# Kernel optimization log

Hardware: AMD Instinct MI355X
Metric: run time of the kernel (lower is better)

Reference implementation:

```python
import jax, jax.numpy as jnp
import numpy as np

B, S, H = 8, 512, 1024          # batch, seq, hidden_size
E = 1024                        # moe_intermediate_size
NEXP, TOPK = 32, 4              # num_experts, top_k_experts
CAP = 512
NH = 4                          # heads in StandardAttentionExpert
HD = E // NH                    # head_dim = 256


def setup_inputs() -> dict:
    key = jax.random.key(0)
    ks = jax.random.split(key, 8)
    def init(k, shape, fan_in):
        return jax.random.normal(k, shape, jnp.float32) / np.sqrt(fan_in)
    return {
        "hidden_states": jax.random.normal(ks[0], (B, S, H), jnp.float32),
        "router_w": init(ks[1], (NEXP, H), H),            # Linear(H, NEXP, bias=False)
        "qkv_w": init(ks[2], (NEXP, 3 * E, H), H),
        "qkv_b": init(ks[3], (NEXP, 3 * E), H),
        "sw_w": init(ks[4], (NEXP, 2 * E, E), E),         # SwiGLU.w
        "sw_b": jnp.zeros((NEXP, 2 * E), jnp.float32),
        "sv_w": init(ks[5], (NEXP, E, E), E),             # SwiGLU.v
        "sv_b": jnp.zeros((NEXP, E), jnp.float32),
        "proj_w": init(ks[6], (NEXP, H, E), E),
        "proj_b": jnp.zeros((NEXP, H), jnp.float32),
    }


def _expert(x, valid, is_linear, qkv_w, qkv_b, sw_w, sw_b, sv_w, sv_b, proj_w, proj_b):
    # x: [CAP, H] padded token group for one expert; valid: [CAP] bool
    qkv = x @ qkv_w.T + qkv_b                      # [CAP, 3E]
    q, k, v = jnp.split(qkv, 3, axis=-1)           # each [CAP, E]
    vm = valid.astype(x.dtype)[:, None]
    # --- LinearAttentionExpert: group-global linear attention ---
    km, vmv = k * vm, v * vm                       # zero out padding keys/values
    kv = km.T @ vmv                                # [E, E]
    z = 1.0 / (q @ km.sum(0) + 1e-6)               # [CAP]
    lin_out = (q @ kv) * z[:, None]                # [CAP, E]
    # --- StandardAttentionExpert: 4-head softmax attention over the group ---
    qh = q.reshape(CAP, NH, HD)
    kh = k.reshape(CAP, NH, HD)
    vh = v.reshape(CAP, NH, HD)
    logits = jnp.einsum('qhd,khd->hqk', qh, kh) / np.sqrt(HD)
    logits = jnp.where(valid[None, None, :], logits, -1e9)
    attn = jax.nn.softmax(logits, axis=-1)
    std_out = jnp.einsum('hqk,khd->qhd', attn, vh).reshape(CAP, E)
    a = jnp.where(is_linear, lin_out, std_out)
    # SwiGLU then projection back to hidden size
    hgl = a @ sw_w.T + sw_b                        # [CAP, 2E]
    u, gate = jnp.split(hgl, 2, axis=-1)
    s = (u * jax.nn.silu(gate)) @ sv_w.T + sv_b    # [CAP, E]
    return s @ proj_w.T + proj_b                   # [CAP, H]


def _forward(hidden_states, router_w, qkv_w, qkv_b, sw_w, sw_b, sv_w, sv_b, proj_w, proj_b):
    T = B * S
    x = hidden_states.reshape(T, H)
    probs = jax.nn.softmax(x @ router_w.T, axis=-1)        # [T, NEXP]
    topw, topi = jax.lax.top_k(probs, TOPK)                # [T, TOPK]
    topw = topw / (topw.sum(-1, keepdims=True) + 1e-6)
    is_linear = (jnp.arange(NEXP) % 4 == 0)
    run = jax.vmap(_expert, in_axes=(0,) * 12 if False else (0, 0, 0, 0, 0, 0, 0, 0, 0, 0, 0))
    out = jnp.zeros_like(x)
    for kk in range(TOPK):
        eid = topi[:, kk]                                  # [T] expert id per token
        oh = (eid[:, None] == jnp.arange(NEXP)).astype(jnp.int32)
        pos = jnp.take_along_axis(jnp.cumsum(oh, axis=0), eid[:, None], axis=1)[:, 0] - 1
        ok = pos < CAP                                     # capacity-drop guard (CAP sized to avoid drops)
        p = jnp.where(ok, pos, CAP)                        # overflow rows land in scratch slot CAP
        buf = jnp.zeros((NEXP, CAP + 1, H), x.dtype).at[eid, p].set(x)[:, :CAP]
        vbuf = jnp.zeros((NEXP, CAP + 1), bool).at[eid, p].set(True)[:, :CAP]
        eo = run(buf, vbuf, is_linear, qkv_w, qkv_b, sw_w, sw_b, sv_w, sv_b, proj_w, proj_b)
        y = jnp.where(ok[:, None], eo[eid, jnp.minimum(pos, CAP - 1)], 0.0)
        out = out + y * topw[:, kk:kk + 1]
    return out.reshape(B, S, H)


def reference(hidden_states, router_w, qkv_w, qkv_b, sw_w, sw_b, sv_w, sv_b, proj_w, proj_b):
    return _forward(hidden_states, router_w, qkv_w, qkv_b, sw_w, sw_b, sv_w, sv_b, proj_w, proj_b)
```

## Files before the change

kernel.cpp:

```cpp
#include <hip/hip_runtime.h>
#include <hip/hip_bf16.h>
#include <cstdint>

#define T_TOK 4096
#define NEXP  32
#define TOPK  4
#define CAP   512
#define H     1024
#define E     1024
#define NH    4
#define HD    256
#define MAXROWS (T_TOK*TOPK)

typedef __attribute__((ext_vector_type(4))) float f32x4;
typedef __attribute__((ext_vector_type(8))) short short8;

__device__ __forceinline__ float bf2f(ushort u) {
  return __uint_as_float(((uint)u) << 16);
}
__device__ __forceinline__ ushort f2bf(float f) {
  uint u = __float_as_uint(f);
  uint r = (u + 0x7fffu + ((u >> 16) & 1u)) >> 16;
  return (ushort)r;
}
__device__ __forceinline__ void split2(float v, ushort& h, ushort& l) {
  h = f2bf(v);
  l = f2bf(v - bf2f(h));
}
__device__ __forceinline__ void gload16(const void* g, void* l) {
  __builtin_amdgcn_global_load_lds((const __attribute__((address_space(1))) void*)g,
                                   (__attribute__((address_space(3))) void*)l, 16, 0, 0);
}

#define CVTPK(F0, F1, HP, LP) do { \
  asm("v_cvt_pk_bf16_f32 %0, %1, %2" : "=v"(HP) : "v"(F0), "v"(F1)); \
  float _h0 = __uint_as_float((HP) << 16); \
  float _h1 = __uint_as_float((HP) & 0xffff0000u); \
  float _l0 = (F0) - _h0, _l1 = (F1) - _h1; \
  asm("v_cvt_pk_bf16_f32 %0, %1, %2" : "=v"(LP) : "v"(_l0), "v"(_l1)); \
} while (0)

#define CVTPK_HI(F0, F1, HP) \
  asm("v_cvt_pk_bf16_f32 %0, %1, %2" : "=v"(HP) : "v"(F0), "v"(F1))

__global__ __launch_bounds__(256) void k_router(const float* __restrict__ x, const float* __restrict__ rw,
                                                int* __restrict__ topi, float* __restrict__ topw) {
  int t = blockIdx.x;
  __shared__ float4 xs[256];
  __shared__ float lg[NEXP];
  const float4* xr = (const float4*)(x + (size_t)t * H);
  xs[threadIdx.x] = xr[threadIdx.x];
  __syncthreads();
  int g = threadIdx.x >> 3, s = threadIdx.x & 7;
  const float4* wr = (const float4*)(rw + (size_t)g * H);
  float acc = 0.f;
  for (int j = s; j < 256; j += 8) {
    float4 a = xs[j], b = wr[j];
    acc += a.x * b.x + a.y * b.y + a.z * b.z + a.w * b.w;
  }
  acc += __shfl_xor(acc, 1);
  acc += __shfl_xor(acc, 2);
  acc += __shfl_xor(acc, 4);
  if (s == 0) lg[g] = acc;
  __syncthreads();
  if (threadIdx.x == 0) {
    float mx = -3e38f;
    for (int j = 0; j < NEXP; j++) mx = fmaxf(mx, lg[j]);
    float p[NEXP]; float sum = 0.f;
    for (int j = 0; j < NEXP; j++) { p[j] = __expf(lg[j] - mx); sum += p[j]; }
    float inv = 1.f / sum;
    int idx[TOPK]; float val[TOPK];
    for (int k = 0; k < TOPK; k++) {
      int best = 0; float bv = -1.f;
      for (int j = 0; j < NEXP; j++) if (p[j] > bv) { bv = p[j]; best = j; }
      idx[k] = best; val[k] = bv * inv; p[best] = -2.f;
    }
    float wsn = val[0] + val[1] + val[2] + val[3] + 1e-6f;
    for (int k = 0; k < TOPK; k++) { topi[t*TOPK + k] = idx[k]; topw[t*TOPK + k] = val[k] / wsn; }
  }
}

__global__ __launch_bounds__(256) void k_scan(const int* __restrict__ topi, int* __restrict__ pos_arr,
                                              int* __restrict__ cnt_raw) {
  int p = blockIdx.x;
  int e = p >> 2, kk = p & 3;
  __shared__ int wtot[4];
  int lane = threadIdx.x & 63, wid = threadIdx.x >> 6;
  int base = 0;
  for (int t0 = 0; t0 < T_TOK; t0 += 256) {
    int t = t0 + threadIdx.x;
    bool flag = (topi[t*TOPK + kk] == e);
    unsigned long long m = __ballot(flag);
    int excl = __popcll(m & ((1ull << lane) - 1ull));
    if (lane == 0) wtot[wid] = __popcll(m);
    __syncthreads();
    int wexcl = 0, tot = 0;
#pragma unroll
    for (int w2 = 0; w2 < 4; w2++) { int v = wtot[w2]; if (w2 < wid) wexcl += v; tot += v; }
    if (flag) pos_arr[t*TOPK + kk] = base + wexcl + excl;
    base += tot;
    __syncthreads();
  }
  if (threadIdx.x == 0) cnt_raw[p] = base;
}

__global__ void k_offsets(const int* __restrict__ cnt_raw, int* __restrict__ cnt,
                          int* __restrict__ row_base, int* __restrict__ meta) {
  if (threadIdx.x == 0 && blockIdx.x == 0) {
    int acc = 0;
    for (int p = 0; p < NEXP*TOPK; p++) {
      int c = cnt_raw[p]; if (c > CAP) c = CAP;
      cnt[p] = c; row_base[p] = acc; acc += c;
    }
    meta[0] = acc;
  }
}

__global__ __launch_bounds__(256) void k_gather(const float* __restrict__ x, const int* __restrict__ topi,
                                                const int* __restrict__ pos_arr, const int* __restrict__ row_base,
                                                int* __restrict__ row_of, ushort* __restrict__ xhi, ushort* __restrict__ xlo) {
  int b = blockIdx.x;
  int t = b >> 2, kk = b & 3;
  int e = topi[b];
  int pos = pos_arr[b];
  int row = (pos < CAP) ? (row_base[e*TOPK + kk] + pos) : -1;
  if (threadIdx.x == 0) row_of[b] = row;
  if (row >= 0) {
    float4 v = ((const float4*)x)[(size_t)t * 256 + threadIdx.x];
    ushort4 h, l;
    split2(v.x, h.x, l.x); split2(v.y, h.y, l.y);
    split2(v.z, h.z, l.z); split2(v.w, h.w, l.w);
    ((ushort4*)xhi)[(size_t)row * 256 + threadIdx.x] = h;
    ((ushort4*)xlo)[(size_t)row * 256 + threadIdx.x] = l;
  }
}

template<int OMODE>
__global__ __launch_bounds__(256) void k_mfma_gemm(
    const ushort* __restrict__ Ahi, const ushort* __restrict__ Alo,
    const float* __restrict__ W, const float* __restrict__ Bias, int Ntot, int n0c,
    float* __restrict__ Cf, ushort* __restrict__ Chi, ushort* __restrict__ Clo, int ldc,
    const int* __restrict__ row_base, const int* __restrict__ cnt, const int* __restrict__ meta) {
  int e = blockIdx.z;
  bool full = (e & 3) == 0;
  int rs = row_base[e*4];
  int re = row_base[e*4 + 3] + cnt[e*4 + 3];
  int m0 = rs + blockIdx.y * 128;
  if (m0 >= re) return;
  int nb = blockIdx.x * 128;
  int tot = meta[0];
  __shared__ ushort ldsA[2][128*32];
  __shared__ float  ldsW[128*32];
  int tid = threadIdx.x;
  int lane = tid & 63, w = tid >> 6;
  int wr = w >> 1, wc = w & 1;
  int lr = lane & 15, lk = lane >> 4;
  f32x4 acc[4][4] = {};

  int r0 = tid >> 2;
  int gA = (tid >> 3) & 3;
  int kc = (((tid & 3) ^ gA)) << 3;
  size_t a_off0 = (size_t)min(m0 + r0, tot - 1) * 1024 + kc;
  size_t a_off1 = (size_t)min(m0 + 64 + r0, tot - 1) * 1024 + kc;
  uint d0 = (uint)tid * 8, d1 = (uint)(256 + tid) * 8;

  const float* wsrc0; const float* wsrc1; const float* wsrc2; const float* wsrc3;
  {
    int i0 = tid;           int rr0 = i0 >> 3, c0 = (i0 & 7) ^ (rr0 & 7);
    int i1 = tid + 256;     int rr1 = i1 >> 3, c1 = (i1 & 7) ^ (rr1 & 7);
    int i2 = tid + 512;     int rr2 = i2 >> 3, c2 = (i2 & 7) ^ (rr2 & 7);
    int i3 = tid + 768;     int rr3 = i3 >> 3, c3 = (i3 & 7) ^ (rr3 & 7);
    wsrc0 = W + ((size_t)e * Ntot + n0c + nb + rr0) * 1024 + c0 * 4;
    wsrc1 = W + ((size_t)e * Ntot + n0c + nb + rr1) * 1024 + c1 * 4;
    wsrc2 = W + ((size_t)e * Ntot + n0c + nb + rr2) * 1024 + c2 * 4;
    wsrc3 = W + ((size_t)e * Ntot + n0c + nb + rr3) * 1024 + c3 * 4;
  }

  for (int kb = 0; kb < 1024; kb += 32) {
    gload16(Ahi + a_off0 + kb, &ldsA[0][d0]);
    gload16(Ahi + a_off1 + kb, &ldsA[0][d1]);
    if (full) {
      gload16(Alo + a_off0 + kb, &ldsA[1][d0]);
      gload16(Alo + a_off1 + kb, &ldsA[1][d1]);
    }
    gload16(wsrc0 + kb, &ldsW[(uint)tid * 4]);
    gload16(wsrc1 + kb, &ldsW[(uint)(tid + 256) * 4]);
    gload16(wsrc2 + kb, &ldsW[(uint)(tid + 512) * 4]);
    gload16(wsrc3 + kb, &ldsW[(uint)(tid + 768) * 4]);
    __syncthreads();
    short8 ah[4], al[4], bh[4], bl[4];
#pragma unroll
    for (int m = 0; m < 4; m++) {
      int rA = wr*64 + m*16 + lr;
      int sA = (lk ^ ((rA >> 1) & 3)) << 3;
      ah[m] = *(const short8*)&ldsA[0][rA*32 + sA];
    }
    if (full) {
#pragma unroll
      for (int m = 0; m < 4; m++) {
        int rA = wr*64 + m*16 + lr;
        int sA = (lk ^ ((rA >> 1) & 3)) << 3;
        al[m] = *(const short8*)&ldsA[1][rA*32 + sA];
      }
#pragma unroll
      for (int n = 0; n < 4; n++) {
        int rB = wc*64 + n*16 + lr;
        int x7 = rB & 7;
        float4 w0 = *(const float4*)&ldsW[rB*32 + (((lk*2)     ^ x7) << 2)];
        float4 w1 = *(const float4*)&ldsW[rB*32 + (((lk*2 + 1) ^ x7) << 2)];
        uint hp0, hp1, hp2, hp3, lp0, lp1, lp2, lp3;
        CVTPK(w0.x, w0.y, hp0, lp0);
        CVTPK(w0.z, w0.w, hp1, lp1);
        CVTPK(w1.x, w1.y, hp2, lp2);
        CVTPK(w1.z, w1.w, hp3, lp3);
        uint4 hv = make_uint4(hp0, hp1, hp2, hp3);
        uint4 lv = make_uint4(lp0, lp1, lp2, lp3);
        bh[n] = __builtin_bit_cast(short8, hv);
        bl[n] = __builtin_bit_cast(short8, lv);
      }
#pragma unroll
      for (int m = 0; m < 4; m++)
#pragma unroll
        for (int n = 0; n < 4; n++) {
          acc[m][n] = __builtin_amdgcn_mfma_f32_16x16x32_bf16(ah[m], bh[n], acc[m][n], 0, 0, 0);
          acc[m][n] = __builtin_amdgcn_mfma_f32_16x16x32_bf16(ah[m], bl[n], acc[m][n], 0, 0, 0);
          acc[m][n] = __builtin_amdgcn_mfma_f32_16x16x32_bf16(al[m], bh[n], acc[m][n], 0, 0, 0);
        }
    } else {
#pragma unroll
      for (int n = 0; n < 4; n++) {
        int rB = wc*64 + n*16 + lr;
        int x7 = rB & 7;
        float4 w0 = *(const float4*)&ldsW[rB*32 + (((lk*2)     ^ x7) << 2)];
        float4 w1 = *(const float4*)&ldsW[rB*32 + (((lk*2 + 1) ^ x7) << 2)];
        uint hp0, hp1, hp2, hp3;
        CVTPK_HI(w0.x, w0.y, hp0);
        CVTPK_HI(w0.z, w0.w, hp1);
        CVTPK_HI(w1.x, w1.y, hp2);
        CVTPK_HI(w1.z, w1.w, hp3);
        uint4 hv = make_uint4(hp0, hp1, hp2, hp3);
        bh[n] = __builtin_bit_cast(short8, hv);
      }
#pragma unroll
      for (int m = 0; m < 4; m++)
#pragma unroll
        for (int n = 0; n < 4; n++)
          acc[m][n] = __builtin_amdgcn_mfma_f32_16x16x32_bf16(ah[m], bh[n], acc[m][n], 0, 0, 0);
    }
    __syncthreads();
  }
#pragma unroll
  for (int n = 0; n < 4; n++) {
    int colG = n0c + nb + wc*64 + n*16 + lr;
    float bi = Bias[(size_t)e * Ntot + colG];
#pragma unroll
    for (int m = 0; m < 4; m++) {
      int rb = m0 + wr*64 + m*16 + lk*4;
#pragma unroll
      for (int g = 0; g < 4; g++) {
        int r = rb + g;
        if (r < re) {
          float v = acc[m][n][g] + bi;
          if constexpr (OMODE == 0) {
            Cf[(size_t)r * ldc + colG] = v;
          } else if constexpr (OMODE == 1) {
            Chi[(size_t)r * ldc + colG] = f2bf(v);
          } else {
            if (full) {
              ushort h, l; split2(v, h, l);
              Chi[(size_t)r * ldc + colG] = h;
              Clo[(size_t)r * ldc + colG] = l;
            } else {
              Chi[(size_t)r * ldc + colG] = f2bf(v);
            }
          }
        }
      }
    }
  }
}

__global__ __launch_bounds__(256) void k_xsum(const ushort* __restrict__ xhi, const ushort* __restrict__ xlo,
                                              const int* __restrict__ row_base, const int* __restrict__ cnt,
                                              float* __restrict__ xsum) {
  int li = blockIdx.x;
  int z = (li >> 2) * 16 + (li & 3);
  int n = cnt[z], base = row_base[z];
  int t = threadIdx.x;
  float a0 = 0.f, a1 = 0.f, a2 = 0.f, a3 = 0.f;
  for (int r = 0; r < n; r++) {
    ushort4 h = ((const ushort4*)(xhi + (size_t)(base + r) * 1024))[t];
    ushort4 l = ((const ushort4*)(xlo + (size_t)(base + r) * 1024))[t];
    a0 += bf2f(h.x) + bf2f(l.x); a1 += bf2f(h.y) + bf2f(l.y);
    a2 += bf2f(h.z) + bf2f(l.z); a3 += bf2f(h.w) + bf2f(l.w);
  }
  float4 o = make_float4(a0, a1, a2, a3);
  ((float4*)(xsum + (size_t)li * 1024))[t] = o;
}

__global__ __launch_bounds__(256) void k_kmv1b(const float* __restrict__ qkvw, const float* __restrict__ qkvb,
                                               const float* __restrict__ xsum, const int* __restrict__ cnt,
                                               float* __restrict__ ksum) {
  int ei = blockIdx.x;
  int e = ei * 4;
  int dblk = blockIdx.y;
  __shared__ float xs[4][1024];
  for (int i = threadIdx.x; i < 4096; i += 256) {
    int sl = i >> 10, h = i & 1023;
    xs[sl][h] = xsum[(size_t)(ei*4 + sl) * 1024 + h];
  }
  __syncthreads();
  int d_loc = threadIdx.x >> 3, hc = threadIdx.x & 7;
  int d = dblk * 32 + d_loc;
  const float* wrow = qkvw + ((size_t)e * 3072 + 1024 + d) * 1024;
  float a0 = 0.f, a1 = 0.f, a2 = 0.f, a3 = 0.f;
  for (int j = 0; j < 8; j++) {
    int h0 = j * 128 + hc * 16;
#pragma unroll
    for (int q = 0; q < 4; q++) {
      float4 wv = *(const float4*)(wrow + h0 + q*4);
#pragma unroll
      for (int b = 0; b < 4; b++) {
        float wf = (b == 0) ? wv.x : (b == 1) ? wv.y : (b == 2) ? wv.z : wv.w;
        int h = h0 + q*4 + b;
        a0 += wf * xs[0][h]; a1 += wf * xs[1][h];
        a2 += wf * xs[2][h]; a3 += wf * xs[3][h];
      }
    }
  }
  for (int m = 1; m < 8; m <<= 1) {
    a0 += __shfl_xor(a0, m); a1 += __shfl_xor(a1, m);
    a2 += __shfl_xor(a2, m); a3 += __shfl_xor(a3, m);
  }
  if (hc == 0) {
    float bk = qkvb[(size_t)e * 3072 + 1024 + d];
#pragma unroll
    for (int sl = 0; sl < 4; sl++) {
      float n = (float)cnt[ei * 16 + sl];
      float v = (sl == 0) ? a0 : (sl == 1) ? a1 : (sl == 2) ? a2 : a3;
      ksum[(size_t)(ei*4 + sl) * 1024 + d] = v + n * bk;
    }
  }
}

__global__ __launch_bounds__(256) void k_kmv2b(const float* __restrict__ qkvw, const float* __restrict__ ksum,
                                               float* __restrict__ upart) {
  int ei = blockIdx.x;
  int hb = blockIdx.y;
  int dc = blockIdx.z;
  int e = ei * 4;
  __shared__ float ks[4][128];
  for (int i = threadIdx.x; i < 512; i += 256) {
    int sl = i >> 7, d = i & 127;
    ks[sl][d] = ksum[(size_t)(ei*4 + sl) * 1024 + dc*128 + d];
  }
  __syncthreads();
  int h = hb * 256 + threadIdx.x;
  float a0 = 0.f, a1 = 0.f, a2 = 0.f, a3 = 0.f;
  const float* wq = qkvw + (size_t)e * 3072 * 1024 + (size_t)(dc * 128) * 1024 + h;
  for (int d = 0; d < 128; d++) {
    float wf = wq[(size_t)d * 1024];
    a0 += wf * ks[0][d]; a1 += wf * ks[1][d];
    a2 += wf * ks[2][d]; a3 += wf * ks[3][d];
  }
  size_t ob = (size_t)(ei*8 + dc) * 4096;
  upart[ob + 0*1024 + h] = a0;
  upart[ob + 1*1024 + h] = a1;
  upart[ob + 2*1024 + h] = a2;
  upart[ob + 3*1024 + h] = a3;
}

__global__ __launch_bounds__(256) void k_kmv2r(const float* __restrict__ upart, float* __restrict__ uvec) {
  int li = blockIdx.x;
  int ei = li >> 2, sl = li & 3;
  int h = blockIdx.y * 256 + threadIdx.x;
  float a = 0.f;
  for (int dc = 0; dc < 8; dc++)
    a += upart[(size_t)(ei*8 + dc) * 4096 + (size_t)sl * 1024 + h];
  uvec[(size_t)li * 1024 + h] = a;
}

__global__ __launch_bounds__(256) void k_cdot(const float* __restrict__ qkvb, const float* __restrict__ ksum,
                                              float* __restrict__ cvec) {
  int li = blockIdx.x;
  int e = (li >> 2) * 4;
  const float* bq = qkvb + (size_t)e * 3072;
  const float* ks = ksum + (size_t)li * 1024;
  float acc = 0.f;
  for (int d = threadIdx.x; d < 1024; d += 256) acc += bq[d] * ks[d];
  __shared__ float red[256];
  red[threadIdx.x] = acc;
  __syncthreads();
  for (int s = 128; s > 0; s >>= 1) {
    if (threadIdx.x < s) red[threadIdx.x] += red[threadIdx.x + s];
    __syncthreads();
  }
  if (threadIdx.x == 0) cvec[li] = red[0];
}

__global__ __launch_bounds__(256) void k_denom(const ushort* __restrict__ xhi, const ushort* __restrict__ xlo,
                                               const float* __restrict__ uvec, const float* __restrict__ cvec,
                                               const int* __restrict__ row_base, const int* __restrict__ cnt,
                                               float* __restrict__ denomArr) {
  int li = blockIdx.y;
  int z = (li >> 2) * 16 + (li & 3);
  int n = cnt[z], base = row_base[z];
  int g = threadIdx.x >> 5, lane = threadIdx.x & 31;
  int r = blockIdx.x * 8 + g;
  if (r >= n) return;
  const ushort* xh = xhi + (size_t)(base + r) * 1024;
  const ushort* xl = xlo + (size_t)(base + r) * 1024;
  const float* u = uvec + (size_t)li * 1024;
  float dn = 0.f;
  for (int j = 0; j < 32; j++) {
    int h = lane + j * 32;
    dn += (bf2f(xh[h]) + bf2f(xl[h])) * u[h];
  }
  dn += __shfl_xor(dn, 1); dn += __shfl_xor(dn, 2); dn += __shfl_xor(dn, 4);
  dn += __shfl_xor(dn, 8); dn += __shfl_xor(dn, 16);
  if (lane == 0) denomArr[base + r] = dn + cvec[li];
}

__global__ __launch_bounds__(256) void k_attn_std(const ushort* __restrict__ qkv,
                                                  ushort* __restrict__ ahi, ushort* __restrict__ alo,
                                                  const int* __restrict__ row_base, const int* __restrict__ cnt,
                                                  const int* __restrict__ meta) {
  int z = blockIdx.z;
  int e = z >> 2;
  if ((e & 3) == 0) return;
  int n = cnt[z];
  int q0 = blockIdx.x * 64;
  if (q0 >= n) return;
  int h = blockIdx.y;
  int base = row_base[z];
  int tot = meta[0];

  __shared__ ushort Kb[32*264];
  __shared__ ushort Vt[256*40];
  __shared__ ushort Pb[4*16*40];

  int tid = threadIdx.x;
  int lane = tid & 63, w = tid >> 6;
  int lr = lane & 15, lk = lane >> 4;

  int qrow = base + q0 + w*16 + lr;
  const ushort* qptr = qkv + (size_t)min(qrow, tot - 1) * 3072 + h*256 + lk*8;
  short8 qf[8];
#pragma unroll
  for (int f = 0; f < 8; f++) qf[f] = *(const short8*)(qptr + f*32);

  f32x4 Oacc[16];
#pragma unroll
  for (int db = 0; db < 16; db++) Oacc[db] = (f32x4){0.f, 0.f, 0.f, 0.f};
  float m_run[4], l_run[4];
#pragma unroll
  for (int g = 0; g < 4; g++) { m_run[g] = -3e38f; l_run[g] = 0.f; }

  int ntile = (n + 31) >> 5;
  for (int t = 0; t < ntile; t++) {
    __syncthreads();
    for (int s = tid; s < 1024; s += 256) {
      int key = s >> 5, ch = s & 31;
      int krow = t*32 + key;
      short8 v = {0,0,0,0,0,0,0,0};
      if (krow < n) v = *(const short8*)(qkv + (size_t)(base + krow)*3072 + 1024 + h*256 + ch*8);
      *(short8*)(Kb + key*264 + ch*8) = v;
    }
    {
      int k2 = tid >> 3, dg = tid & 7;
      bool kval = (t*32 + k2) < n;
      const ushort* vsrc = qkv + (size_t)(base + min(t*32 + k2, n - 1))*3072 + 2048 + h*256 + dg*8;
#pragma unroll
      for (int tt = 0; tt < 4; tt++) {
        int dd = dg*8 + tt*64;
        short8 v = {0,0,0,0,0,0,0,0};
        if (kval) v = *(const short8*)(vsrc + tt*64);
#pragma unroll
        for (int j = 0; j < 8; j++) Vt[(dd + j)*40 + k2] = ((ushort*)&v)[j];
      }
    }
    __syncthreads();
    f32x4 S0 = (f32x4){0.f,0.f,0.f,0.f}, S1 = (f32x4){0.f,0.f,0.f,0.f};
#pragma unroll
    for (int db = 0; db < 8; db++) {
      short8 b0 = *(const short8*)(Kb + lr*264 + db*32 + lk*8);
      short8 b1 = *(const short8*)(Kb + (16 + lr)*264 + db*32 + lk*8);
      S0 = __builtin_amdgcn_mfma_f32_16x16x32_bf16(qf[db], b0, S0, 0, 0, 0);
      S1 = __builtin_amdgcn_mfma_f32_16x16x32_bf16(qf[db], b1, S1, 0, 0, 0);
    }
    bool v0 = (t*32 + lr) < n, v1 = (t*32 + 16 + lr) < n;
    float p0v[4], p1v[4], scv[4];
#pragma unroll
    for (int g = 0; g < 4; g++) {
      float s0 = v0 ? S0[g] * 0.0625f : -1e9f;
      float s1 = v1 ? S1[g] * 0.0625f : -1e9f;
      float mx = fmaxf(s0, s1);
      mx = fmaxf(mx, __shfl_xor(mx, 1)); mx = fmaxf(mx, __shfl_xor(mx, 2));
      mx = fmaxf(mx, __shfl_xor(mx, 4)); mx = fmaxf(mx, __shfl_xor(mx, 8));
      float nm = fmaxf(m_run[g], mx);
      float sc = __expf(m_run[g] - nm);
      m_run[g] = nm;
      float p0 = __expf(s0 - nm), p1 = __expf(s1 - nm);
      float sum = p0 + p1;
      sum += __shfl_xor(sum, 1); sum += __shfl_xor(sum, 2);
      sum += __shfl_xor(sum, 4); sum += __shfl_xor(sum, 8);
      l_run[g] = l_run[g] * sc + sum;
      p0v[g] = p0; p1v[g] = p1; scv[g] = sc;
    }
#pragma unroll
    for (int db = 0; db < 16; db++)
#pragma unroll
      for (int g = 0; g < 4; g++) Oacc[db][g] *= scv[g];
    ushort* pw = Pb + w*640;
#pragma unroll
    for (int g = 0; g < 4; g++) {
      int q = lk*4 + g;
      pw[q*40 + lr] = f2bf(p0v[g]);
      pw[q*40 + 16 + lr] = f2bf(p1v[g]);
    }
    __syncthreads();
    short8 pa = *(const short8*)(pw + lr*40 + lk*8);
#pragma unroll
    for (int db = 0; db < 16; db++) {
      short8 vb = *(const short8*)(Vt + (db*16 + lr)*40 + lk*8);
      Oacc[db] = __builtin_amdgcn_mfma_f32_16x16x32_bf16(pa, vb, Oacc[db], 0, 0, 0);
    }
  }
#pragma unroll
  for (int g = 0; g < 4; g++) {
    int qr = q0 + w*16 + lk*4 + g;
    if (qr < n) {
      float inv = 1.f / l_run[g];
      size_t ro = (size_t)(base + qr) * 1024 + h*256;
#pragma unroll
      for (int db = 0; db < 16; db++) {
        float v = Oacc[db][g] * inv;
        ushort hh, ll; split2(v, hh, ll);
        ahi[ro + db*16 + lr] = hh;
        alo[ro + db*16 + lr] = ll;
      }
    }
  }
}

__global__ __launch_bounds__(256) void k_lin_qkt(const ushort* __restrict__ qkv,
                                                 ushort* __restrict__ Shi, ushort* __restrict__ Slo,
                                                 const int* __restrict__ row_base, const int* __restrict__ cnt) {
  int li = blockIdx.z;
  int z = (li >> 2) * 16 + (li & 3);
  int n = cnt[z];
  int q0 = blockIdx.y * 128, k0 = blockIdx.x * 128;
  if (q0 >= n || k0 >= n) return;
  int base = row_base[z];
  __shared__ ushort lds[2][128*32];
  int tid = threadIdx.x;
  int lane = tid & 63, w = tid >> 6;
  int wr = w >> 1, wc = w & 1;
  int lr = lane & 15, lk = lane >> 4;
  f32x4 acc[4][4] = {};
  int r0 = tid >> 2;
  int kc = (tid & 3) << 3;
  size_t a0 = (size_t)(base + min(q0 + r0, n - 1)) * 3072 + kc;
  size_t a1 = (size_t)(base + min(q0 + 64 + r0, n - 1)) * 3072 + kc;
  size_t b0 = (size_t)(base + min(k0 + r0, n - 1)) * 3072 + 1024 + kc;
  size_t b1 = (size_t)(base + min(k0 + 64 + r0, n - 1)) * 3072 + 1024 + kc;
  uint d0 = (uint)tid * 8, d1 = (uint)(256 + tid) * 8;
  for (int kb = 0; kb < 1024; kb += 32) {
    gload16(qkv + a0 + kb, &lds[0][d0]);
    gload16(qkv + a1 + kb, &lds[0][d1]);
    gload16(qkv + b0 + kb, &lds[1][d0]);
    gload16(qkv + b1 + kb, &lds[1][d1]);
    __syncthreads();
    short8 af[4], bf[4];
#pragma unroll
    for (int m = 0; m < 4; m++) af[m] = *(const short8*)&lds[0][(wr*64 + m*16 + lr)*32 + lk*8];
#pragma unroll
    for (int n2 = 0; n2 < 4; n2++) bf[n2] = *(const short8*)&lds[1][(wc*64 + n2*16 + lr)*32 + lk*8];
#pragma unroll
    for (int m = 0; m < 4; m++)
#pragma unroll
      for (int n2 = 0; n2 < 4; n2++)
        acc[m][n2] = __builtin_amdgcn_mfma_f32_16x16x32_bf16(af[m], bf[n2], acc[m][n2], 0, 0, 0);
    __syncthreads();
  }
#pragma unroll
  for (int n2 = 0; n2 < 4; n2++) {
    int col = k0 + wc*64 + n2*16 + lr;
#pragma unroll
    for (int m = 0; m < 4; m++) {
#pragma unroll
      for (int g = 0; g < 4; g++) {
        int row = q0 + wr*64 + m*16 + lk*4 + g;
        if (row < n) {
          float v = (col < n) ? acc[m][n2][g] : 0.f;
          ushort hh, ll; split2(v, hh, ll);
          size_t o = (size_t)li * (CAP*CAP) + (size_t)row * CAP + col;
          Shi[o] = hh; Slo[o] = ll;
        }
      }
    }
  }
}

__global__ __launch_bounds__(256) void k_lin_pv(const ushort* __restrict__ qkv,
                                                const ushort* __restrict__ Shi, const ushort* __restrict__ Slo,
                                                ushort* __restrict__ ahi, ushort* __restrict__ alo,
                                                const int* __restrict__ row_base, const int* __restrict__ cnt,
                                                const float* __restrict__ denomArr) {
  int li = blockIdx.y;
  int z = (li >> 2) * 16 + (li & 3);
  int n = cnt[z];
  int q0 = blockIdx.x * 64;
  if (q0 >= n) return;
  int base = row_base[z];
  __shared__ ushort Vt[256*40];
  int tid = threadIdx.x;
  int lane = tid & 63, w = tid >> 6;
  int lr = lane & 15, lk = lane >> 4;
  int ntile = (n + 31) >> 5;
  int k2 = tid >> 3, dg = tid & 7;
  int qrow = min(q0 + w*16 + lr, n - 1);
  const ushort* srowH = Shi + (size_t)li * (CAP*CAP) + (size_t)qrow * CAP;
  const ushort* srowL = Slo + (size_t)li * (CAP*CAP) + (size_t)qrow * CAP;
  for (int c = 0; c < 4; c++) {
    f32x4 Oacc[16];
#pragma unroll
    for (int db = 0; db < 16; db++) Oacc[db] = (f32x4){0.f, 0.f, 0.f, 0.f};
    for (int t = 0; t < ntile; t++) {
      __syncthreads();
      int krow = t*32 + k2;
      bool kval = krow < n;
      const ushort* vsrc = qkv + (size_t)(base + min(krow, n - 1))*3072 + 2048 + c*256 + dg*8;
#pragma unroll
      for (int tt = 0; tt < 4; tt++) {
        int dd = dg*8 + tt*64;
        short8 v = {0,0,0,0,0,0,0,0};
        if (kval) v = *(const short8*)(vsrc + tt*64);
#pragma unroll
        for (int j = 0; j < 8; j++) Vt[(dd + j)*40 + k2] = ((ushort*)&v)[j];
      }
      __syncthreads();
      short8 ph = *(const short8*)(srowH + t*32 + lk*8);
      short8 pl = *(const short8*)(srowL + t*32 + lk*8);
#pragma unroll
      for (int db = 0; db < 16; db++) {
        short8 vb = *(const short8*)(Vt + (db*16 + lr)*40 + lk*8);
        Oacc[db] = __builtin_amdgcn_mfma_f32_16x16x32_bf16(ph, vb, Oacc[db], 0, 0, 0);
        Oacc[db] = __builtin_amdgcn_mfma_f32_16x16x32_bf16(pl, vb, Oacc[db], 0, 0, 0);
      }
    }
#pragma unroll
    for (int g = 0; g < 4; g++) {
      int qr = q0 + w*16 + lk*4 + g;
      if (qr < n) {
        float zq = 1.f / (denomArr[base + qr] + 1e-6f);
        size_t ro = (size_t)(base + qr) * 1024 + c*256;
#pragma unroll
        for (int db = 0; db < 16; db++) {
          float v = Oacc[db][g] * zq;
          ushort hh, ll; split2(v, hh, ll);
          ahi[ro + db*16 + lr] = hh;
          alo[ro + db*16 + lr] = ll;
        }
      }
    }
  }
}

__global__ __launch_bounds__(256) void k_silu(const float* __restrict__ hgl, ushort* __restrict__ ghi,
                                              ushort* __restrict__ glo, const int* __restrict__ meta) {
  int r = blockIdx.x;
  if (r >= meta[0]) return;
  const float4* u4 = (const float4*)(hgl + (size_t)r * 2048);
  float4 u = u4[threadIdx.x];
  float4 gt = u4[256 + threadIdx.x];
  float4 o;
  o.x = u.x * (gt.x / (1.f + __expf(-gt.x)));
  o.y = u.y * (gt.y / (1.f + __expf(-gt.y)));
  o.z = u.z * (gt.z / (1.f + __expf(-gt.z)));
  o.w = u.w * (gt.w / (1.f + __expf(-gt.w)));
  ushort4 h, l;
  split2(o.x, h.x, l.x); split2(o.y, h.y, l.y);
  split2(o.z, h.z, l.z); split2(o.w, h.w, l.w);
  ((ushort4*)ghi)[(size_t)r * 256 + threadIdx.x] = h;
  ((ushort4*)glo)[(size_t)r * 256 + threadIdx.x] = l;
}

__global__ __launch_bounds__(256) void k_scatter(const float* __restrict__ o, const int* __restrict__ row_of,
                                                 const float* __restrict__ topw, float* __restrict__ out) {
  int t = blockIdx.x;
  float4 acc = make_float4(0.f, 0.f, 0.f, 0.f);
  for (int k = 0; k < TOPK; k++) {
    int row = row_of[t*TOPK + k];
    if (row >= 0) {
      float w = topw[t*TOPK + k];
      float4 v = ((const float4*)o)[(size_t)row * 256 + threadIdx.x];
      acc.x += w * v.x; acc.y += w * v.y; acc.z += w * v.z; acc.w += w * v.w;
    }
  }
  ((float4*)out)[(size_t)t * 256 + threadIdx.x] = acc;
}

extern "C" void kernel_launch(void* const* d_in, const int* in_sizes, int n_in,
                              void* d_out, int out_size, void* d_ws, size_t ws_size,
                              hipStream_t stream) {
  const float* x    = (const float*)d_in[0];
  const float* rw   = (const float*)d_in[1];
  const float* qkvw = (const float*)d_in[2];
  const float* qkvb = (const float*)d_in[3];
  const float* sww  = (const float*)d_in[4];
  const float* swb  = (const float*)d_in[5];
  const float* svw  = (const float*)d_in[6];
  const float* svb  = (const float*)d_in[7];
  const float* pjw  = (const float*)d_in[8];
  const float* pjb  = (const float*)d_in[9];
  float* out = (float*)d_out;

  char* ws = (char*)d_ws;
  const size_t MB = 1ull << 20;
  ushort* xhi  = (ushort*)(ws + 0);
  ushort* xlo  = (ushort*)(ws + 32*MB);
  ushort* qkvB = (ushort*)(ws + 64*MB);
  ushort* ahi  = (ushort*)(ws + 160*MB);
  ushort* alo  = (ushort*)(ws + 192*MB);
  ushort* Shi  = (ushort*)(ws + 224*MB);
  ushort* Slo  = (ushort*)(ws + 240*MB);
  float*  hgl  = (float*)(ws + 0);
  ushort* ghi  = ahi;
  ushort* glo  = alo;
  ushort* shi  = (ushort*)(ws + 0);
  ushort* slo  = (ushort*)(ws + 32*MB);
  float*  obuf = (float*)(ws + 64*MB);
  char* sm = ws + 288*MB;
  size_t off = 0;
  auto alloc = [&](size_t bytes) { char* p = sm + off; off += (bytes + 255) & ~(size_t)255; return p; };
  int*   topi = (int*)alloc(T_TOK*TOPK*4);
  float* topw = (float*)alloc(T_TOK*TOPK*4);
  int*   pos  = (int*)alloc(T_TOK*TOPK*4);
  int*   rof  = (int*)alloc(T_TOK*TOPK*4);
  int*   craw = (int*)alloc(NEXP*TOPK*4);
  int*   cnt  = (int*)alloc(NEXP*TOPK*4);
  int*   rbase= (int*)alloc(NEXP*TOPK*4);
  int*   meta = (int*)alloc(256);
  float* xsum = (float*)alloc(32*1024*4);
  float* ksum = (float*)alloc(32*1024*4);
  float* uvec = (float*)alloc(32*1024*4);
  float* cvec = (float*)alloc(32*4);
  float* denomArr = (float*)alloc(MAXROWS*4);
  float* upart = (float*)alloc(8*8*4*1024*4);

  k_router <<<T_TOK, 256, 0, stream>>>(x, rw, topi, topw);
  k_scan   <<<NEXP*TOPK, 256, 0, stream>>>(topi, pos, craw);
  k_offsets<<<1, 64, 0, stream>>>(craw, cnt, rbase, meta);
  k_gather <<<T_TOK*TOPK, 256, 0, stream>>>(x, topi, pos, rbase, rof, xhi, xlo);

  k_xsum  <<<32, 256, 0, stream>>>(xhi, xlo, rbase, cnt, xsum);
  k_kmv1b <<<dim3(8, 32), 256, 0, stream>>>(qkvw, qkvb, xsum, cnt, ksum);
  k_kmv2b <<<dim3(8, 4, 8), 256, 0, stream>>>(qkvw, ksum, upart);
  k_kmv2r <<<dim3(32, 4), 256, 0, stream>>>(upart, uvec);
  k_cdot  <<<32, 256, 0, stream>>>(qkvb, ksum, cvec);
  k_denom <<<dim3(64, 32), 256, 0, stream>>>(xhi, xlo, uvec, cvec, rbase, cnt, denomArr);

  dim3 gqkv(3072/128, 16, NEXP);
  k_mfma_gemm<1><<<gqkv, 256, 0, stream>>>(xhi, xlo, qkvw, qkvb, 3072, 0,
                                           nullptr, qkvB, nullptr, 3072, rbase, cnt, meta);

  dim3 ga(CAP/64, NH, NEXP*TOPK);
  k_attn_std<<<ga, 256, 0, stream>>>(qkvB, ahi, alo, rbase, cnt, meta);
  dim3 gq(CAP/128, CAP/128, 32);
  k_lin_qkt<<<gq, 256, 0, stream>>>(qkvB, Shi, Slo, rbase, cnt);
  dim3 gp(CAP/64, 32);
  k_lin_pv<<<gp, 256, 0, stream>>>(qkvB, Shi, Slo, ahi, alo, rbase, cnt, denomArr);

  dim3 gsw(2048/128, 16, NEXP);
  k_mfma_gemm<0><<<gsw, 256, 0, stream>>>(ahi, alo, sww, swb, 2048, 0,
                                          hgl, nullptr, nullptr, 2048, rbase, cnt, meta);
  k_silu<<<MAXROWS, 256, 0, stream>>>(hgl, ghi, glo, meta);

  dim3 g1k(1024/128, 16, NEXP);
  k_mfma_gemm<2><<<g1k, 256, 0, stream>>>(ghi, glo, svw, svb, 1024, 0,
                                          nullptr, shi, slo, 1024, rbase, cnt, meta);
  k_mfma_gemm<0><<<g1k, 256, 0, stream>>>(shi, slo, pjw, pjb, 1024, 0,
                                          obuf, nullptr, nullptr, 1024, rbase, cnt, meta);

  k_scatter<<<T_TOK, 256, 0, stream>>>(obuf, rof, topw, out);
}
```

Before: 1.548 ms.

## Double-buffer LDS tiles in MFMA expert GEMM to overlap loads with compute

Splits the A (hi/lo bf16) and fp32 W shared-memory tiles into two buffers. The loop now prefetches the next K-slice into the alternate buffer while running MFMAs on the current one, so global-to-LDS latency overlaps with compute. This doubles the LDS footprint per block, to 64KB, which can lower the number of resident blocks per CU.

```diff
diff --git a/kernel.cpp b/kernel.cpp
--- a/kernel.cpp
+++ b/kernel.cpp
@@ -149,8 +149,8 @@
   if (m0 >= re) return;
   int nb = blockIdx.x * 128;
   int tot = meta[0];
-  __shared__ ushort ldsA[2][128*32];
-  __shared__ float  ldsW[128*32];
+  __shared__ ushort ldsA[2][2][128*32];
+  __shared__ float  ldsW[2][128*32];
   int tid = threadIdx.x;
   int lane = tid & 63, w = tid >> 6;
   int wr = w >> 1, wc = w & 1;
@@ -176,38 +176,48 @@
     wsrc3 = W + ((size_t)e * Ntot + n0c + nb + rr3) * 1024 + c3 * 4;
   }
 
-  for (int kb = 0; kb < 1024; kb += 32) {
-    gload16(Ahi + a_off0 + kb, &ldsA[0][d0]);
-    gload16(Ahi + a_off1 + kb, &ldsA[0][d1]);
+  auto STAGE = [&](int buf, int kb) {
+    gload16(Ahi + a_off0 + kb, &ldsA[buf][0][d0]);
+    gload16(Ahi + a_off1 + kb, &ldsA[buf][0][d1]);
     if (full) {
-      gload16(Alo + a_off0 + kb, &ldsA[1][d0]);
-      gload16(Alo + a_off1 + kb, &ldsA[1][d1]);
-    }
-    gload16(wsrc0 + kb, &ldsW[(uint)tid * 4]);
-    gload16(wsrc1 + kb, &ldsW[(uint)(tid + 256) * 4]);
-    gload16(wsrc2 + kb, &ldsW[(uint)(tid + 512) * 4]);
-    gload16(wsrc3 + kb, &ldsW[(uint)(tid + 768) * 4]);
-    __syncthreads();
+      gload16(Alo + a_off0 + kb, &ldsA[buf][1][d0]);
+      gload16(Alo + a_off1 + kb, &ldsA[buf][1][d1]);
+    }
+    gload16(wsrc0 + kb, &ldsW[buf][(uint)tid * 4]);
+    gload16(wsrc1 + kb, &ldsW[buf][(uint)(tid + 256) * 4]);
+    gload16(wsrc2 + kb, &ldsW[buf][(uint)(tid + 512) * 4]);
+    gload16(wsrc3 + kb, &ldsW[buf][(uint)(tid + 768) * 4]);
+  };
+
+  STAGE(0, 0);
+  __syncthreads();
+
+  for (int kt = 0; kt < 32; kt++) {
+    int cur = kt & 1;
+    if (kt < 31) STAGE(cur ^ 1, (kt + 1) * 32);
+    const ushort* aHi = ldsA[cur][0];
+    const ushort* aLo = ldsA[cur][1];
+    const float*  wL  = ldsW[cur];
     short8 ah[4], al[4], bh[4], bl[4];
 #pragma unroll
     for (int m = 0; m < 4; m++) {
       int rA = wr*64 + m*16 + lr;
       int sA = (lk ^ ((rA >> 1) & 3)) << 3;
-      ah[m] = *(const short8*)&ldsA[0][rA*32 + sA];
+      ah[m] = *(const short8*)&aHi[rA*32 + sA];
     }
     if (full) {
 #pragma unroll
       for (int m = 0; m < 4; m++) {
         int rA = wr*64 + m*16 + lr;
         int sA = (lk ^ ((rA >> 1) & 3)) << 3;
-        al[m] = *(const short8*)&ldsA[1][rA*32 + sA];
+        al[m] = *(const short8*)&aLo[rA*32 + sA];
       }
 #pragma unroll
       for (int n = 0; n < 4; n++) {
         int rB = wc*64 + n*16 + lr;
         int x7 = rB & 7;
-        float4 w0 = *(const float4*)&ldsW[rB*32 + (((lk*2)     ^ x7) << 2)];
-        float4 w1 = *(const float4*)&ldsW[rB*32 + (((lk*2 + 1) ^ x7) << 2)];
+        float4 w0 = *(const float4*)&wL[rB*32 + (((lk*2)     ^ x7) << 2)];
+        float4 w1 = *(const float4*)&wL[rB*32 + (((lk*2 + 1) ^ x7) << 2)];
         uint hp0, hp1, hp2, hp3, lp0, lp1, lp2, lp3;
         CVTPK(w0.x, w0.y, hp0, lp0);
         CVTPK(w0.z, w0.w, hp1, lp1);
@@ -231,8 +241,8 @@
       for (int n = 0; n < 4; n++) {
         int rB = wc*64 + n*16 + lr;
         int x7 = rB & 7;
-        float4 w0 = *(const float4*)&ldsW[rB*32 + (((lk*2)     ^ x7) << 2)];
-        float4 w1 = *(const float4*)&ldsW[rB*32 + (((lk*2 + 1) ^ x7) << 2)];
+        float4 w0 = *(const float4*)&wL[rB*32 + (((lk*2)     ^ x7) << 2)];
+        float4 w1 = *(const float4*)&wL[rB*32 + (((lk*2 + 1) ^ x7) << 2)];
         uint hp0, hp1, hp2, hp3;
         CVTPK_HI(w0.x, w0.y, hp0);
         CVTPK_HI(w0.z, w0.w, hp1);
```

After: 1.541 ms. Within noise of the previous version (-0.4%).

## Enlarge expert GEMM tile to 256 rows with each wave covering all 128 columns

Applied to the files above, without the earlier changes.

The grouped MFMA GEMM tile grows from 128x128 to 256x128. Each of the four waves now owns 64 rows across all 128 columns, so W tiles are loaded and converted to bf16 once per 256 rows instead of once per 128. This halves redundant fp32 weight traffic and hi/lo splitting per output, at the cost of doubled accumulator registers, more LDS for A, and half as many blocks in the grid. Each B fragment is now consumed right after conversion, interleaved with the MFMAs.

```diff
diff --git a/kernel.cpp b/kernel.cpp
--- a/kernel.cpp
+++ b/kernel.cpp
@@ -145,66 +145,63 @@
   bool full = (e & 3) == 0;
   int rs = row_base[e*4];
   int re = row_base[e*4 + 3] + cnt[e*4 + 3];
-  int m0 = rs + blockIdx.y * 128;
+  int m0 = rs + blockIdx.y * 256;
   if (m0 >= re) return;
   int nb = blockIdx.x * 128;
   int tot = meta[0];
-  __shared__ ushort ldsA[2][128*32];
+  __shared__ ushort ldsA[2][256*32];
   __shared__ float  ldsW[128*32];
   int tid = threadIdx.x;
-  int lane = tid & 63, w = tid >> 6;
-  int wr = w >> 1, wc = w & 1;
+  int lane = tid & 63, wv = tid >> 6;
   int lr = lane & 15, lk = lane >> 4;
-  f32x4 acc[4][4] = {};
-
-  int r0 = tid >> 2;
-  int gA = (tid >> 3) & 3;
-  int kc = (((tid & 3) ^ gA)) << 3;
-  size_t a_off0 = (size_t)min(m0 + r0, tot - 1) * 1024 + kc;
-  size_t a_off1 = (size_t)min(m0 + 64 + r0, tot - 1) * 1024 + kc;
-  uint d0 = (uint)tid * 8, d1 = (uint)(256 + tid) * 8;
-
-  const float* wsrc0; const float* wsrc1; const float* wsrc2; const float* wsrc3;
-  {
-    int i0 = tid;           int rr0 = i0 >> 3, c0 = (i0 & 7) ^ (rr0 & 7);
-    int i1 = tid + 256;     int rr1 = i1 >> 3, c1 = (i1 & 7) ^ (rr1 & 7);
-    int i2 = tid + 512;     int rr2 = i2 >> 3, c2 = (i2 & 7) ^ (rr2 & 7);
-    int i3 = tid + 768;     int rr3 = i3 >> 3, c3 = (i3 & 7) ^ (rr3 & 7);
-    wsrc0 = W + ((size_t)e * Ntot + n0c + nb + rr0) * 1024 + c0 * 4;
-    wsrc1 = W + ((size_t)e * Ntot + n0c + nb + rr1) * 1024 + c1 * 4;
-    wsrc2 = W + ((size_t)e * Ntot + n0c + nb + rr2) * 1024 + c2 * 4;
-    wsrc3 = W + ((size_t)e * Ntot + n0c + nb + rr3) * 1024 + c3 * 4;
+  f32x4 acc[4][8] = {};
+
+  int rowA = tid >> 2;
+  int kc = (((tid & 3) ^ ((tid >> 3) & 3))) << 3;
+  size_t a_off[4];
+#pragma unroll
+  for (int q = 0; q < 4; q++)
+    a_off[q] = (size_t)min(m0 + rowA + 64*q, tot - 1) * 1024 + kc;
+
+  const float* wsrc[4];
+#pragma unroll
+  for (int q = 0; q < 4; q++) {
+    int i = tid + 256*q;
+    int rr = i >> 3, c = (i & 7) ^ (rr & 7);
+    wsrc[q] = W + ((size_t)e * Ntot + n0c + nb + rr) * 1024 + c * 4;
   }
 
   for (int kb = 0; kb < 1024; kb += 32) {
-    gload16(Ahi + a_off0 + kb, &ldsA[0][d0]);
-    gload16(Ahi + a_off1 + kb, &ldsA[0][d1]);
+#pragma unroll
+    for (int q = 0; q < 4; q++)
+      gload16(Ahi + a_off[q] + kb, &ldsA[0][(uint)(tid + 256*q) * 8]);
     if (full) {
-      gload16(Alo + a_off0 + kb, &ldsA[1][d0]);
-      gload16(Alo + a_off1 + kb, &ldsA[1][d1]);
-    }
-    gload16(wsrc0 + kb, &ldsW[(uint)tid * 4]);
-    gload16(wsrc1 + kb, &ldsW[(uint)(tid + 256) * 4]);
-    gload16(wsrc2 + kb, &ldsW[(uint)(tid + 512) * 4]);
-    gload16(wsrc3 + kb, &ldsW[(uint)(tid + 768) * 4]);
-    __syncthreads();
-    short8 ah[4], al[4], bh[4], bl[4];
+#pragma unroll
+      for (int q = 0; q < 4; q++)
+        gload16(Alo + a_off[q] + kb, &ldsA[1][(uint)(tid + 256*q) * 8]);
+    }
+#pragma unroll
+    for (int q = 0; q < 4; q++)
+      gload16(wsrc[q] + kb, &ldsW[(uint)(tid + 256*q) * 4]);
+    __syncthreads();
+
+    short8 ah[4], al[4];
 #pragma unroll
     for (int m = 0; m < 4; m++) {
-      int rA = wr*64 + m*16 + lr;
+      int rA = wv*64 + m*16 + lr;
       int sA = (lk ^ ((rA >> 1) & 3)) << 3;
       ah[m] = *(const short8*)&ldsA[0][rA*32 + sA];
     }
     if (full) {
 #pragma unroll
       for (int m = 0; m < 4; m++) {
-        int rA = wr*64 + m*16 + lr;
+        int rA = wv*64 + m*16 + lr;
         int sA = (lk ^ ((rA >> 1) & 3)) << 3;
         al[m] = *(const short8*)&ldsA[1][rA*32 + sA];
       }
 #pragma unroll
-      for (int n = 0; n < 4; n++) {
-        int rB = wc*64 + n*16 + lr;
+      for (int n = 0; n < 8; n++) {
+        int rB = n*16 + lr;
         int x7 = rB & 7;
         float4 w0 = *(const float4*)&ldsW[rB*32 + (((lk*2)     ^ x7) << 2)];
         float4 w1 = *(const float4*)&ldsW[rB*32 + (((lk*2 + 1) ^ x7) << 2)];
@@ -215,21 +212,19 @@
         CVTPK(w1.z, w1.w, hp3, lp3);
         uint4 hv = make_uint4(hp0, hp1, hp2, hp3);
         uint4 lv = make_uint4(lp0, lp1, lp2, lp3);
-        bh[n] = __builtin_bit_cast(short8, hv);
-        bl[n] = __builtin_bit_cast(short8, lv);
-      }
-#pragma unroll
-      for (int m = 0; m < 4; m++)
-#pragma unroll
-        for (int n = 0; n < 4; n++) {
-          acc[m][n] = __builtin_amdgcn_mfma_f32_16x16x32_bf16(ah[m], bh[n], acc[m][n], 0, 0, 0);
-          acc[m][n] = __builtin_amdgcn_mfma_f32_16x16x32_bf16(ah[m], bl[n], acc[m][n], 0, 0, 0);
-          acc[m][n] = __builtin_amdgcn_mfma_f32_16x16x32_bf16(al[m], bh[n], acc[m][n], 0, 0, 0);
+        short8 bh = __builtin_bit_cast(short8, hv);
+        short8 bl = __builtin_bit_cast(short8, lv);
+#pragma unroll
+        for (int m = 0; m < 4; m++) {
+          acc[m][n] = __builtin_amdgcn_mfma_f32_16x16x32_bf16(ah[m], bh, acc[m][n], 0, 0, 0);
+          acc[m][n] = __builtin_amdgcn_mfma_f32_16x16x32_bf16(ah[m], bl, acc[m][n], 0, 0, 0);
+          acc[m][n] = __builtin_amdgcn_mfma_f32_16x16x32_bf16(al[m], bh, acc[m][n], 0, 0, 0);
         }
+      }
     } else {
 #pragma unroll
-      for (int n = 0; n < 4; n++) {
-        int rB = wc*64 + n*16 + lr;
+      for (int n = 0; n < 8; n++) {
+        int rB = n*16 + lr;
         int x7 = rB & 7;
         float4 w0 = *(const float4*)&ldsW[rB*32 + (((lk*2)     ^ x7) << 2)];
         float4 w1 = *(const float4*)&ldsW[rB*32 + (((lk*2 + 1) ^ x7) << 2)];
@@ -239,23 +234,21 @@
         CVTPK_HI(w1.x, w1.y, hp2);
         CVTPK_HI(w1.z, w1.w, hp3);
         uint4 hv = make_uint4(hp0, hp1, hp2, hp3);
-        bh[n] = __builtin_bit_cast(short8, hv);
-      }
-#pragma unroll
-      for (int m = 0; m < 4; m++)
-#pragma unroll
-        for (int n = 0; n < 4; n++)
-          acc[m][n] = __builtin_amdgcn_mfma_f32_16x16x32_bf16(ah[m], bh[n], acc[m][n], 0, 0, 0);
-    }
-    __syncthreads();
-  }
-#pragma unroll
-  for (int n = 0; n < 4; n++) {
-    int colG = n0c + nb + wc*64 + n*16 + lr;
+        short8 bh = __builtin_bit_cast(short8, hv);
+#pragma unroll
+        for (int m = 0; m < 4; m++)
+          acc[m][n] = __builtin_amdgcn_mfma_f32_16x16x32_bf16(ah[m], bh, acc[m][n], 0, 0, 0);
+      }
+    }
+    __syncthreads();
+  }
+#pragma unroll
+  for (int n = 0; n < 8; n++) {
+    int colG = n0c + nb + n*16 + lr;
     float bi = Bias[(size_t)e * Ntot + colG];
 #pragma unroll
     for (int m = 0; m < 4; m++) {
-      int rb = m0 + wr*64 + m*16 + lk*4;
+      int rb = m0 + wv*64 + m*16 + lk*4;
 #pragma unroll
       for (int g = 0; g < 4; g++) {
         int r = rb + g;
@@ -761,7 +754,7 @@
   k_cdot  <<<32, 256, 0, stream>>>(qkvb, ksum, cvec);
   k_denom <<<dim3(64, 32), 256, 0, stream>>>(xhi, xlo, uvec, cvec, rbase, cnt, denomArr);
 
-  dim3 gqkv(3072/128, 16, NEXP);
+  dim3 gqkv(3072/128, 8, NEXP);
   k_mfma_gemm<1><<<gqkv, 256, 0, stream>>>(xhi, xlo, qkvw, qkvb, 3072, 0,
                                            nullptr, qkvB, nullptr, 3072, rbase, cnt, meta);
 
@@ -772,12 +765,12 @@
   dim3 gp(CAP/64, 32);
   k_lin_pv<<<gp, 256, 0, stream>>>(qkvB, Shi, Slo, ahi, alo, rbase, cnt, denomArr);
 
-  dim3 gsw(2048/128, 16, NEXP);
+  dim3 gsw(2048/128, 8, NEXP);
   k_mfma_gemm<0><<<gsw, 256, 0, stream>>>(ahi, alo, sww, swb, 2048, 0,
                                           hgl, nullptr, nullptr, 2048, rbase, cnt, meta);
   k_silu<<<MAXROWS, 256, 0, stream>>>(hgl, ghi, glo, meta);
 
-  dim3 g1k(1024/128, 16, NEXP);
+  dim3 g1k(1024/128, 8, NEXP);
   k_mfma_gemm<2><<<g1k, 256, 0, stream>>>(ghi, glo, svw, svb, 1024, 0,
                                           nullptr, shi, slo, 1024, rbase, cnt, meta);
   k_mfma_gemm<0><<<g1k, 256, 0, stream>>>(shi, slo, pjw, pjb, 1024, 0,
```

Result: slower. 2.351 ms (+51.9%).
